# Performance work log

Measured on AMD Instinct MI355X. Metric: run time of the kernel, lower is better.

Reference implementation:

```python
import jax, jax.numpy as jnp
import numpy as np
import math

B, C, L = 16, 2048, 64

def setup_inputs() -> dict:
    key = jax.random.key(0)
    kq, kk, kv = jax.random.split(key, 3)
    q = jax.random.normal(kq, (B, C, L), dtype=jnp.float32)
    k = jax.random.normal(kk, (B, C, L), dtype=jnp.float32)
    v = jax.random.normal(kv, (B, C, L), dtype=jnp.float32)
    return {"q": q, "k": k, "v": v}

def reference(q, k, v):
    b, c, l = q.shape
    # Faithful to the torch source: k is RESHAPED (row-major), not transposed.
    k_t = k.reshape(b, l, c)                      # (b, l, c)
    score = jnp.matmul(q, k_t) / math.sqrt(l)     # (b, c, c)
    # nn.Softmax() with no dim on a 3D tensor -> torch implicit dim = 0 (batch axis)
    score = jax.nn.softmax(score, axis=0)
    return jnp.matmul(score, v)                   # (b, c, l)
```

## Files before the change

kernel.cpp:

```cpp
#include <hip/hip_runtime.h>

typedef __attribute__((ext_vector_type(8))) short short8;
typedef __attribute__((ext_vector_type(4))) float float4v;

#define BATCH 16
#define CDIM 2048
#define LDIM 64
#define BSTRIDE (CDIM * LDIM)

__device__ __forceinline__ float bf2f(unsigned short u) {
    return __uint_as_float(((unsigned int)u) << 16);
}
__device__ __forceinline__ unsigned short f2bf(float f) {
    unsigned int x = __float_as_uint(f);
    x += 0x7fffu + ((x >> 16) & 1u);
    return (unsigned short)(x >> 16);
}
__device__ __forceinline__ void dma16(const void* g, void* l) {
    __builtin_amdgcn_global_load_lds(
        (const __attribute__((address_space(1))) void*)g,
        (__attribute__((address_space(3))) void*)l, 16, 0, 0);
}

__global__ __launch_bounds__(256) void prepass_kernel(
    const float* __restrict__ q, const float* __restrict__ k, const float* __restrict__ v,
    float* __restrict__ out, unsigned short* __restrict__ qb,
    unsigned short* __restrict__ kT, unsigned short* __restrict__ vS)
{
    __shared__ unsigned short T[64][68];
    const int bx = blockIdx.x;
    const int t = threadIdx.x;

    if (bx < 1024) {
        float4v z = (float4v){0.f, 0.f, 0.f, 0.f};
        float4v* o = (float4v*)out + (size_t)bx * 512 + t * 2;
        o[0] = z; o[1] = z;
    } else if (bx < 2048) {
        int i = (bx - 1024) * 256 + t;
        const float4v* src = (const float4v*)q + (size_t)i * 2;
        float4v x0 = src[0], x1 = src[1];
        unsigned int u0 = f2bf(x0[0] * 0.125f) | ((unsigned)f2bf(x0[1] * 0.125f) << 16);
        unsigned int u1 = f2bf(x0[2] * 0.125f) | ((unsigned)f2bf(x0[3] * 0.125f) << 16);
        unsigned int u2 = f2bf(x1[0] * 0.125f) | ((unsigned)f2bf(x1[1] * 0.125f) << 16);
        unsigned int u3 = f2bf(x1[2] * 0.125f) | ((unsigned)f2bf(x1[3] * 0.125f) << 16);
        int b = i >> 14, r = i & 16383, m = r >> 3, j = r & 7;
        *(uint4*)(qb + (size_t)b * BSTRIDE + m * 64 + (j ^ (m & 7)) * 8) =
            make_uint4(u0, u1, u2, u3);
    } else if (bx < 2560) {
        int idx = bx - 2048, b = idx >> 5, n0 = (idx & 31) * 64;
        const float* src = k + (size_t)b * BSTRIDE + (size_t)(t >> 2) * 2048 + n0 + (t & 3) * 16;
#pragma unroll
        for (int kk = 0; kk < 4; kk++) {
            float4v x = *(const float4v*)(src + kk * 4);
#pragma unroll
            for (int e = 0; e < 4; e++)
                T[t >> 2][(t & 3) * 16 + kk * 4 + e] = f2bf(x[e]);
        }
        __syncthreads();
        unsigned short* dst = kT + (size_t)b * BSTRIDE;
        int n = t & 63;
#pragma unroll
        for (int jj = 0; jj < 2; jj++) {
            int j = (t >> 6) * 2 + jj;
            ushort4 g0, g1;
#pragma unroll
            for (int e = 0; e < 4; e++) { g0[e] = T[j * 8 + e][n]; g1[e] = T[j * 8 + 4 + e][n]; }
            *(uint4*)(dst + (size_t)(n0 + n) * 64 + (j ^ (n & 7)) * 8) =
                make_uint4(g0.x | ((unsigned)g0.y << 16), g0.z | ((unsigned)g0.w << 16),
                           g1.x | ((unsigned)g1.y << 16), g1.z | ((unsigned)g1.w << 16));
        }
    } else {
        int idx = bx - 2560, b = idx >> 5, n0 = (idx & 31) * 64;
        const float* src = v + (size_t)b * BSTRIDE + (size_t)(t >> 2) * 64 + n0 * 0 + (t & 3) * 16;
        src += (size_t)n0 * 64;
#pragma unroll
        for (int kk = 0; kk < 4; kk++) {
            float4v x = *(const float4v*)(src + kk * 4);
#pragma unroll
            for (int e = 0; e < 4; e++)
                T[t >> 2][(t & 3) * 16 + kk * 4 + e] = f2bf(x[e]);
        }
        __syncthreads();
        unsigned short* dst = vS + (size_t)b * BSTRIDE;
        int j = t & 63, qc = t >> 6;
#pragma unroll
        for (int nb = 0; nb < 2; nb++) {
            ushort4 g0, g1;
#pragma unroll
            for (int e = 0; e < 4; e++) {
                g0[e] = T[nb * 32 + qc * 8 + e][j];
                g1[e] = T[nb * 32 + qc * 8 + 4 + e][j];
            }
            *(uint4*)(dst + (size_t)(n0 / 32 + nb) * 2048 + j * 32 + (qc ^ (j & 3)) * 8) =
                make_uint4(g0.x | ((unsigned)g0.y << 16), g0.z | ((unsigned)g0.w << 16),
                           g1.x | ((unsigned)g1.y << 16), g1.z | ((unsigned)g1.w << 16));
        }
    }
}

__global__ __launch_bounds__(256, 2) void dinv_kernel(
    const unsigned short* __restrict__ qb, const unsigned short* __restrict__ kT,
    unsigned short* __restrict__ Dt)
{
    __shared__ unsigned short Sq[2][8192];
    __shared__ unsigned short Sk[2][4096];
    const int tid = threadIdx.x, w = tid >> 6, lane = tid & 63;
    const int c = lane & 15, q = lane >> 4;
    const int mt = blockIdx.x & 15, ng = blockIdx.x >> 4;
    const int m0 = mt * 128, n0 = ng * 64;

    float4v Dacc[2][4];
#pragma unroll
    for (int ms = 0; ms < 2; ms++)
#pragma unroll
        for (int nt = 0; nt < 4; nt++) Dacc[ms][nt] = (float4v){0.f, 0.f, 0.f, 0.f};

    {
        const char* qg = (const char*)(qb + (size_t)m0 * 64);
        const char* kg = (const char*)(kT + (size_t)n0 * 64);
#pragma unroll
        for (int kk = 0; kk < 4; kk++)
            dma16(qg + (w * 4 + kk) * 1024 + lane * 16, (char*)Sq[0] + (w * 4 + kk) * 1024);
        dma16(kg + (w * 2 + 0) * 1024 + lane * 16, (char*)Sk[0] + (w * 2 + 0) * 1024);
        dma16(kg + (w * 2 + 1) * 1024 + lane * 16, (char*)Sk[0] + (w * 2 + 1) * 1024);
    }

    for (int bb = 0; bb < BATCH; bb++) {
        const int p = bb & 1;
        if (bb < BATCH - 1) {
            const char* qg = (const char*)(qb + (size_t)(bb + 1) * BSTRIDE + (size_t)m0 * 64);
            const char* kg = (const char*)(kT + (size_t)(bb + 1) * BSTRIDE + (size_t)n0 * 64);
#pragma unroll
            for (int kk = 0; kk < 4; kk++)
                dma16(qg + (w * 4 + kk) * 1024 + lane * 16, (char*)Sq[p ^ 1] + (w * 4 + kk) * 1024);
            dma16(kg + (w * 2 + 0) * 1024 + lane * 16, (char*)Sk[p ^ 1] + (w * 2 + 0) * 1024);
            dma16(kg + (w * 2 + 1) * 1024 + lane * 16, (char*)Sk[p ^ 1] + (w * 2 + 1) * 1024);
            asm volatile("s_waitcnt vmcnt(6)" ::: "memory");
        } else {
            asm volatile("s_waitcnt vmcnt(0)" ::: "memory");
        }
        asm volatile("s_barrier" ::: "memory");

        short8 Qf[2][2];
#pragma unroll
        for (int ms = 0; ms < 2; ms++)
#pragma unroll
            for (int h = 0; h < 2; h++)
                Qf[ms][h] = *(const short8*)&Sq[p][(w * 32 + ms * 16 + c) * 64 +
                                                  ((h * 4 + q) ^ (c & 7)) * 8];
#pragma unroll
        for (int nt = 0; nt < 4; nt++) {
            short8 A0 = *(const short8*)&Sk[p][(nt * 16 + c) * 64 + (q ^ (c & 7)) * 8];
            short8 A1 = *(const short8*)&Sk[p][(nt * 16 + c) * 64 + ((4 + q) ^ (c & 7)) * 8];
#pragma unroll
            for (int ms = 0; ms < 2; ms++) {
                float4v d = (float4v){0.f, 0.f, 0.f, 0.f};
                d = __builtin_amdgcn_mfma_f32_16x16x32_bf16(A0, Qf[ms][0], d, 0, 0, 0);
                d = __builtin_amdgcn_mfma_f32_16x16x32_bf16(A1, Qf[ms][1], d, 0, 0, 0);
#pragma unroll
                for (int r = 0; r < 4; r++) Dacc[ms][nt][r] += __expf(d[r]);
            }
        }
        asm volatile("s_barrier" ::: "memory");
    }

#pragma unroll
    for (int ms = 0; ms < 2; ms++)
#pragma unroll
        for (int nt = 0; nt < 4; nt++) {
            unsigned int x = f2bf(1.f / Dacc[ms][nt][0]) |
                             ((unsigned)f2bf(1.f / Dacc[ms][nt][1]) << 16);
            unsigned int y = f2bf(1.f / Dacc[ms][nt][2]) |
                             ((unsigned)f2bf(1.f / Dacc[ms][nt][3]) << 16);
            size_t T = (size_t)(mt * 64 + ng * 2 + (nt >> 1));
            *(uint2*)((char*)Dt + T * 8192 + w * 2048 + (ms * 2 + (nt & 1)) * 512 + lane * 8) =
                make_uint2(x, y);
        }
}

__global__ __launch_bounds__(256, 4) void attn_main_kernel(
    const unsigned short* __restrict__ qb, const unsigned short* __restrict__ kT,
    const unsigned short* __restrict__ vS, const unsigned short* __restrict__ Dt,
    float* __restrict__ out)
{
    __shared__ unsigned short Sk[2][2048];
    __shared__ unsigned short Sv[2][2048];
    __shared__ unsigned short Ep[4][2][16][40];

    const int tid = threadIdx.x, w = tid >> 6, lane = tid & 63;
    const int c = lane & 15, q = lane >> 4;
    const int b = blockIdx.x & 15, mt = (blockIdx.x >> 4) & 15, ns = blockIdx.x >> 8;
    const int m0 = mt * 128, nbase = ns * 512;

    const unsigned short* qb_b = qb + (size_t)b * BSTRIDE;
    const char* kbase = (const char*)(kT + (size_t)b * BSTRIDE);
    const char* vbase = (const char*)(vS + (size_t)b * BSTRIDE);

    short8 Qf[2][2];
#pragma unroll
    for (int ms = 0; ms < 2; ms++)
#pragma unroll
        for (int h = 0; h < 2; h++)
            Qf[ms][h] = *(const short8*)(qb_b + (m0 + w * 32 + ms * 16 + c) * 64 +
                                         ((h * 4 + q) ^ (c & 7)) * 8);
    float4v acc[2][4];
#pragma unroll
    for (int ms = 0; ms < 2; ms++)
#pragma unroll
        for (int jt = 0; jt < 4; jt++) acc[ms][jt] = (float4v){0.f, 0.f, 0.f, 0.f};

    dma16(kbase + (size_t)nbase * 128 + w * 1024 + lane * 16, (char*)Sk[0] + w * 1024);
    dma16(vbase + (size_t)(ns * 16) * 4096 + w * 1024 + lane * 16, (char*)Sv[0] + w * 1024);

    for (int st = 0; st < 16; st++) {
        const int p = st & 1;
        if (st < 15) {
            const int n1 = nbase + (st + 1) * 32;
            dma16(kbase + (size_t)n1 * 128 + w * 1024 + lane * 16, (char*)Sk[p ^ 1] + w * 1024);
            dma16(vbase + (size_t)(ns * 16 + st + 1) * 4096 + w * 1024 + lane * 16,
                  (char*)Sv[p ^ 1] + w * 1024);
            asm volatile("s_waitcnt vmcnt(2)" ::: "memory");
        } else {
            asm volatile("s_waitcnt vmcnt(0)" ::: "memory");
        }
        asm volatile("s_barrier" ::: "memory");

        const char* dtb = (const char*)Dt + (size_t)(mt * 64 + ns * 16 + st) * 8192 +
                          w * 2048 + lane * 8;
        uint2 du[2][2];
        du[0][0] = *(const uint2*)(dtb + 0);
        du[0][1] = *(const uint2*)(dtb + 512);
        du[1][0] = *(const uint2*)(dtb + 1024);
        du[1][1] = *(const uint2*)(dtb + 1536);

#pragma unroll
        for (int nt = 0; nt < 2; nt++) {
            short8 A0 = *(const short8*)&Sk[p][(nt * 16 + c) * 64 + (q ^ (c & 7)) * 8];
            short8 A1 = *(const short8*)&Sk[p][(nt * 16 + c) * 64 + ((4 + q) ^ (c & 7)) * 8];
#pragma unroll
            for (int ms = 0; ms < 2; ms++) {
                float4v d = (float4v){0.f, 0.f, 0.f, 0.f};
                d = __builtin_amdgcn_mfma_f32_16x16x32_bf16(A0, Qf[ms][0], d, 0, 0, 0);
                d = __builtin_amdgcn_mfma_f32_16x16x32_bf16(A1, Qf[ms][1], d, 0, 0, 0);
                uint2 u2 = du[ms][nt];
                ushort4 e;
                e.x = f2bf(__expf(d[0]) * __uint_as_float(u2.x << 16));
                e.y = f2bf(__expf(d[1]) * __uint_as_float(u2.x & 0xffff0000u));
                e.z = f2bf(__expf(d[2]) * __uint_as_float(u2.y << 16));
                e.w = f2bf(__expf(d[3]) * __uint_as_float(u2.y & 0xffff0000u));
                *(ushort4*)&Ep[w][ms][c][nt * 16 + q * 4] = e;
            }
        }
        asm volatile("s_waitcnt lgkmcnt(0)" ::: "memory");

        short8 Vf[4];
#pragma unroll
        for (int jt = 0; jt < 4; jt++)
            Vf[jt] = *(const short8*)&Sv[p][(jt * 16 + c) * 32 + (q ^ (c & 3)) * 8];
#pragma unroll
        for (int ms = 0; ms < 2; ms++) {
            short8 Pf = *(const short8*)&Ep[w][ms][c][q * 8];
#pragma unroll
            for (int jt = 0; jt < 4; jt++)
                acc[ms][jt] = __builtin_amdgcn_mfma_f32_16x16x32_bf16(Pf, Vf[jt], acc[ms][jt], 0, 0, 0);
        }
        asm volatile("s_barrier" ::: "memory");
    }

#pragma unroll
    for (int ms = 0; ms < 2; ms++)
#pragma unroll
        for (int jt = 0; jt < 4; jt++)
#pragma unroll
            for (int r = 0; r < 4; r++) {
                int m = m0 + w * 32 + ms * 16 + q * 4 + r;
                atomicAdd(&out[((size_t)b * CDIM + m) * LDIM + jt * 16 + c], acc[ms][jt][r]);
            }
}

extern "C" void kernel_launch(void* const* d_in, const int* in_sizes, int n_in,
                              void* d_out, int out_size, void* d_ws, size_t ws_size,
                              hipStream_t stream) {
    const float* q = (const float*)d_in[0];
    const float* k = (const float*)d_in[1];
    const float* v = (const float*)d_in[2];
    float* out = (float*)d_out;

    unsigned short* qb = (unsigned short*)d_ws;
    unsigned short* kT = qb + (size_t)BATCH * BSTRIDE;
    unsigned short* vS = kT + (size_t)BATCH * BSTRIDE;
    unsigned short* Dt = vS + (size_t)BATCH * BSTRIDE;

    prepass_kernel<<<3072, 256, 0, stream>>>(q, k, v, out, qb, kT, vS);
    dinv_kernel<<<512, 256, 0, stream>>>(qb, kT, Dt);
    attn_main_kernel<<<1024, 256, 0, stream>>>(qb, kT, vS, Dt, out);
}
```

Measured before the change: 140.7 us.

## Merge N-split blocks into one 1024-thread block with LDS reduction instead of atomics

The four N-split blocks per (batch, M-tile) become one 1024-thread block of 16 waves, where each group of four waves handles a different N slice with its own K/V LDS buffers. Partial outputs are summed in shared memory in four serialized rounds and written with plain vector stores. This removes the zero-init pass over the output in the prepass and all the float atomicAdds to global memory. In exchange there are only 256 blocks, more LDS per block, and the block-wide barriers inside the loop now synchronize all 16 waves, which may cost latency hiding.

```diff
diff --git a/kernel.cpp b/kernel.cpp
--- a/kernel.cpp
+++ b/kernel.cpp
@@ -24,7 +24,7 @@
 
 __global__ __launch_bounds__(256) void prepass_kernel(
     const float* __restrict__ q, const float* __restrict__ k, const float* __restrict__ v,
-    float* __restrict__ out, unsigned short* __restrict__ qb,
+    unsigned short* __restrict__ qb,
     unsigned short* __restrict__ kT, unsigned short* __restrict__ vS)
 {
     __shared__ unsigned short T[64][68];
@@ -32,11 +32,7 @@
     const int t = threadIdx.x;
 
     if (bx < 1024) {
-        float4v z = (float4v){0.f, 0.f, 0.f, 0.f};
-        float4v* o = (float4v*)out + (size_t)bx * 512 + t * 2;
-        o[0] = z; o[1] = z;
-    } else if (bx < 2048) {
-        int i = (bx - 1024) * 256 + t;
+        int i = bx * 256 + t;
         const float4v* src = (const float4v*)q + (size_t)i * 2;
         float4v x0 = src[0], x1 = src[1];
         unsigned int u0 = f2bf(x0[0] * 0.125f) | ((unsigned)f2bf(x0[1] * 0.125f) << 16);
@@ -46,8 +42,8 @@
         int b = i >> 14, r = i & 16383, m = r >> 3, j = r & 7;
         *(uint4*)(qb + (size_t)b * BSTRIDE + m * 64 + (j ^ (m & 7)) * 8) =
             make_uint4(u0, u1, u2, u3);
-    } else if (bx < 2560) {
-        int idx = bx - 2048, b = idx >> 5, n0 = (idx & 31) * 64;
+    } else if (bx < 1536) {
+        int idx = bx - 1024, b = idx >> 5, n0 = (idx & 31) * 64;
         const float* src = k + (size_t)b * BSTRIDE + (size_t)(t >> 2) * 2048 + n0 + (t & 3) * 16;
 #pragma unroll
         for (int kk = 0; kk < 4; kk++) {
@@ -70,9 +66,9 @@
                            g1.x | ((unsigned)g1.y << 16), g1.z | ((unsigned)g1.w << 16));
         }
     } else {
-        int idx = bx - 2560, b = idx >> 5, n0 = (idx & 31) * 64;
-        const float* src = v + (size_t)b * BSTRIDE + (size_t)(t >> 2) * 64 + n0 * 0 + (t & 3) * 16;
-        src += (size_t)n0 * 64;
+        int idx = bx - 1536, b = idx >> 5, n0 = (idx & 31) * 64;
+        const float* src = v + (size_t)b * BSTRIDE + (size_t)n0 * 64 +
+                           (size_t)(t >> 2) * 64 + (t & 3) * 16;
 #pragma unroll
         for (int kk = 0; kk < 4; kk++) {
             float4v x = *(const float4v*)(src + kk * 4);
@@ -178,19 +174,21 @@
         }
 }
 
-__global__ __launch_bounds__(256, 4) void attn_main_kernel(
+__global__ __launch_bounds__(1024, 4) void attn_main_kernel(
     const unsigned short* __restrict__ qb, const unsigned short* __restrict__ kT,
     const unsigned short* __restrict__ vS, const unsigned short* __restrict__ Dt,
     float* __restrict__ out)
 {
-    __shared__ unsigned short Sk[2][2048];
-    __shared__ unsigned short Sv[2][2048];
-    __shared__ unsigned short Ep[4][2][16][40];
+    __shared__ unsigned short Sk[4][2][2048];
+    __shared__ unsigned short Sv[4][2][2048];
+    __shared__ unsigned short Ep[16][2][16][40];
 
     const int tid = threadIdx.x, w = tid >> 6, lane = tid & 63;
     const int c = lane & 15, q = lane >> 4;
-    const int b = blockIdx.x & 15, mt = (blockIdx.x >> 4) & 15, ns = blockIdx.x >> 8;
-    const int m0 = mt * 128, nbase = ns * 512;
+    const int g = w >> 2, ns = w & 3;
+    const int b = blockIdx.x & 15, mt = blockIdx.x >> 4;
+    const int m0 = mt * 128 + g * 32;
+    const int nbase = ns * 512;
 
     const unsigned short* qb_b = qb + (size_t)b * BSTRIDE;
     const char* kbase = (const char*)(kT + (size_t)b * BSTRIDE);
@@ -201,7 +199,7 @@
     for (int ms = 0; ms < 2; ms++)
 #pragma unroll
         for (int h = 0; h < 2; h++)
-            Qf[ms][h] = *(const short8*)(qb_b + (m0 + w * 32 + ms * 16 + c) * 64 +
+            Qf[ms][h] = *(const short8*)(qb_b + (m0 + ms * 16 + c) * 64 +
                                          ((h * 4 + q) ^ (c & 7)) * 8);
     float4v acc[2][4];
 #pragma unroll
@@ -209,16 +207,16 @@
 #pragma unroll
         for (int jt = 0; jt < 4; jt++) acc[ms][jt] = (float4v){0.f, 0.f, 0.f, 0.f};
 
-    dma16(kbase + (size_t)nbase * 128 + w * 1024 + lane * 16, (char*)Sk[0] + w * 1024);
-    dma16(vbase + (size_t)(ns * 16) * 4096 + w * 1024 + lane * 16, (char*)Sv[0] + w * 1024);
+    dma16(kbase + (size_t)nbase * 128 + g * 1024 + lane * 16, (char*)Sk[ns][0] + g * 1024);
+    dma16(vbase + (size_t)(ns * 16) * 4096 + g * 1024 + lane * 16, (char*)Sv[ns][0] + g * 1024);
 
     for (int st = 0; st < 16; st++) {
         const int p = st & 1;
         if (st < 15) {
             const int n1 = nbase + (st + 1) * 32;
-            dma16(kbase + (size_t)n1 * 128 + w * 1024 + lane * 16, (char*)Sk[p ^ 1] + w * 1024);
-            dma16(vbase + (size_t)(ns * 16 + st + 1) * 4096 + w * 1024 + lane * 16,
-                  (char*)Sv[p ^ 1] + w * 1024);
+            dma16(kbase + (size_t)n1 * 128 + g * 1024 + lane * 16, (char*)Sk[ns][p ^ 1] + g * 1024);
+            dma16(vbase + (size_t)(ns * 16 + st + 1) * 4096 + g * 1024 + lane * 16,
+                  (char*)Sv[ns][p ^ 1] + g * 1024);
             asm volatile("s_waitcnt vmcnt(2)" ::: "memory");
         } else {
             asm volatile("s_waitcnt vmcnt(0)" ::: "memory");
@@ -226,7 +224,7 @@
         asm volatile("s_barrier" ::: "memory");
 
         const char* dtb = (const char*)Dt + (size_t)(mt * 64 + ns * 16 + st) * 8192 +
-                          w * 2048 + lane * 8;
+                          g * 2048 + lane * 8;
         uint2 du[2][2];
         du[0][0] = *(const uint2*)(dtb + 0);
         du[0][1] = *(const uint2*)(dtb + 512);
@@ -235,8 +233,8 @@
 
 #pragma unroll
         for (int nt = 0; nt < 2; nt++) {
-            short8 A0 = *(const short8*)&Sk[p][(nt * 16 + c) * 64 + (q ^ (c & 7)) * 8];
-            short8 A1 = *(const short8*)&Sk[p][(nt * 16 + c) * 64 + ((4 + q) ^ (c & 7)) * 8];
+            short8 A0 = *(const short8*)&Sk[ns][p][(nt * 16 + c) * 64 + (q ^ (c & 7)) * 8];
+            short8 A1 = *(const short8*)&Sk[ns][p][(nt * 16 + c) * 64 + ((4 + q) ^ (c & 7)) * 8];
 #pragma unroll
             for (int ms = 0; ms < 2; ms++) {
                 float4v d = (float4v){0.f, 0.f, 0.f, 0.f};
@@ -256,7 +254,7 @@
         short8 Vf[4];
 #pragma unroll
         for (int jt = 0; jt < 4; jt++)
-            Vf[jt] = *(const short8*)&Sv[p][(jt * 16 + c) * 32 + (q ^ (c & 3)) * 8];
+            Vf[jt] = *(const short8*)&Sv[ns][p][(jt * 16 + c) * 32 + (q ^ (c & 3)) * 8];
 #pragma unroll
         for (int ms = 0; ms < 2; ms++) {
             short8 Pf = *(const short8*)&Ep[w][ms][c][q * 8];
@@ -267,15 +265,34 @@
         asm volatile("s_barrier" ::: "memory");
     }
 
-#pragma unroll
-    for (int ms = 0; ms < 2; ms++)
-#pragma unroll
-        for (int jt = 0; jt < 4; jt++)
-#pragma unroll
-            for (int r = 0; r < 4; r++) {
-                int m = m0 + w * 32 + ms * 16 + q * 4 + r;
-                atomicAdd(&out[((size_t)b * CDIM + m) * LDIM + jt * 16 + c], acc[ms][jt][r]);
-            }
+    float* Racc = (float*)&Sk[0][0][0];
+    float* Rg = Racc + g * 2176;
+    __syncthreads();
+#pragma unroll 1
+    for (int round = 0; round < 4; round++) {
+        if (ns == round) {
+#pragma unroll
+            for (int ms = 0; ms < 2; ms++)
+#pragma unroll
+                for (int jt = 0; jt < 4; jt++)
+#pragma unroll
+                    for (int r = 0; r < 4; r++) {
+                        int idx = (ms * 16 + q * 4 + r) * 68 + jt * 16 + c;
+                        if (round == 0) Rg[idx] = acc[ms][jt][r];
+                        else Rg[idx] += acc[ms][jt][r];
+                    }
+        }
+        __syncthreads();
+    }
+    {
+        int mrow = tid >> 3, col0 = (tid & 7) * 8;
+        const float* src = Racc + (mrow >> 5) * 2176 + (mrow & 31) * 68 + col0;
+        float4v v0 = *(const float4v*)(src);
+        float4v v1 = *(const float4v*)(src + 4);
+        float* dst = out + ((size_t)b * CDIM + mt * 128 + mrow) * LDIM + col0;
+        *(float4v*)(dst) = v0;
+        *(float4v*)(dst + 4) = v1;
+    }
 }
 
 extern "C" void kernel_launch(void* const* d_in, const int* in_sizes, int n_in,
@@ -291,7 +308,7 @@
     unsigned short* vS = kT + (size_t)BATCH * BSTRIDE;
     unsigned short* Dt = vS + (size_t)BATCH * BSTRIDE;
 
-    prepass_kernel<<<3072, 256, 0, stream>>>(q, k, v, out, qb, kT, vS);
+    prepass_kernel<<<2048, 256, 0, stream>>>(q, k, v, qb, kT, vS);
     dinv_kernel<<<512, 256, 0, stream>>>(qb, kT, Dt);
-    attn_main_kernel<<<1024, 256, 0, stream>>>(qb, kT, vS, Dt, out);
-}
+    attn_main_kernel<<<256, 1024, 0, stream>>>(qb, kT, vS, Dt, out);
+}
```

New measurement: 129.6 us. 1.08x faster.
